# Performance work log

Hardware: AMD Instinct MI355X
Metric: run time of the kernel (lower is better)

Reference implementation:

```python
import jax, jax.numpy as jnp
import numpy as np

NUM_HEAD = 8
GN_GROUPS = 32
EPS = 1e-5


def group_norm(x, w, b):
    # x: [B,C,H,W]; GroupNorm over 32 groups
    B, C, H, W = x.shape
    xg = x.reshape(B, GN_GROUPS, C // GN_GROUPS, H, W)
    mu = jnp.mean(xg, axis=(2, 3, 4), keepdims=True)
    var = jnp.var(xg, axis=(2, 3, 4), keepdims=True)
    xn = ((xg - mu) * jax.lax.rsqrt(var + EPS)).reshape(B, C, H, W)
    return xn * w[None, :, None, None] + b[None, :, None, None]


def conv1x1(x, w, b):
    # 1x1 conv == channel-wise linear: w [O,C], x [B,C,H,W]
    return jnp.einsum('oc,bchw->bohw', w, x) + b[None, :, None, None]


def setup_inputs() -> dict:
    key = jax.random.key(0)
    ks = jax.random.split(key, 6)
    B, C, H, W = 8, 512, 32, 32
    s = 1.0 / np.sqrt(C)
    return {
        'x': jax.random.normal(ks[0], (B, C, H, W), jnp.float32),
        'gn_w': jnp.ones((C,), jnp.float32),
        'gn_b': jnp.zeros((C,), jnp.float32),
        'wq': jax.random.normal(ks[1], (C, C), jnp.float32) * s,
        'bq': jnp.zeros((C,), jnp.float32),
        'wk': jax.random.normal(ks[2], (C, C), jnp.float32) * s,
        'bk': jnp.zeros((C,), jnp.float32),
        'wv': jax.random.normal(ks[3], (C, C), jnp.float32) * s,
        'bv': jnp.zeros((C,), jnp.float32),
        'wo': jax.random.normal(ks[4], (C, C), jnp.float32) * s,
        'bo': jnp.zeros((C,), jnp.float32),
    }


def reference(x, gn_w, gn_b, wq, bq, wk, bk, wv, bv, wo, bo):
    B, C, H, W = x.shape
    Hn = NUM_HEAD
    d = C // Hn
    N = H * W
    scale = d ** -0.5

    xn = group_norm(x, gn_w, gn_b)
    q = conv1x1(xn, wq, bq).reshape(B, Hn, d, N)  # [B,Hn,d,N]
    k = conv1x1(xn, wk, bk).reshape(B, Hn, d, N)
    v = conv1x1(xn, wv, bv).reshape(B, Hn, d, N)

    # attn[b,h,i,j] = sum_d q[b,h,d,i] * k[b,h,d,j]
    attn = jnp.einsum('bhdi,bhdj->bhij', q, k) * scale
    attn = jax.nn.softmax(attn, axis=-1)
    # out[b,h,d,i] = sum_j attn[b,h,i,j] * v[b,h,d,j]
    out = jnp.einsum('bhij,bhdj->bhdi', attn, v).reshape(B, C, H, W)
    return x + conv1x1(out, wo, bo)
```

## Files before the change

### kernel.cpp

```cpp
#include <hip/hip_runtime.h>
#include <hip/hip_bf16.h>

typedef unsigned short ushort_t;
typedef __bf16 bf16_t;
typedef bf16_t bf16x8 __attribute__((ext_vector_type(8)));
typedef float f32x4 __attribute__((ext_vector_type(4)));

#define CH 512
#define NSP 1024

__device__ __forceinline__ float bf2f(ushort_t u) {
    union { unsigned int i; float f; } t; t.i = ((unsigned int)u) << 16; return t.f;
}
__device__ __forceinline__ ushort_t f2bf(float f) {
    union { float fl; unsigned int i; } t; t.fl = f;
    unsigned int r = t.i + 0x7fffu + ((t.i >> 16) & 1u);
    return (ushort_t)(r >> 16);
}
__device__ __forceinline__ unsigned int pk2(float a, float b) {
    __hip_bfloat162 h = __float22bfloat162_rn(make_float2(a, b));
    union { __hip_bfloat162 h2; unsigned int u; } t; t.h2 = h; return t.u;
}

#if __has_builtin(__builtin_amdgcn_global_load_lds)
#define HAVE_ASYNC_LDS 1
#endif
__device__ __forceinline__ void cp16(const ushort_t* g, ushort_t* l) {
#ifdef HAVE_ASYNC_LDS
    __builtin_amdgcn_global_load_lds((const __attribute__((address_space(1))) unsigned int*)g,
                                     (__attribute__((address_space(3))) unsigned int*)l, 16, 0, 0);
#else
    *(uint4*)l = *(const uint4*)g;
#endif
}

#define QSCALE 0.18033688011112042f

__global__ __launch_bounds__(256) void prep_kernel(const float* __restrict__ x,
                                                   const float* __restrict__ w0, const float* __restrict__ w1,
                                                   const float* __restrict__ w2, const float* __restrict__ w3,
                                                   float2* __restrict__ gstats, ushort_t* __restrict__ wbf) {
    int tid = threadIdx.x;
    if (blockIdx.x >= 256) {
        int idx = (blockIdx.x - 256) * 256 + tid;
        int my = idx >> 16;
        const float* src = (my == 0) ? w0 : (my == 1) ? w1 : (my == 2) ? w2 : w3;
        float4 v = reinterpret_cast<const float4*>(src)[idx & 65535];
        uint2 u = make_uint2(pk2(v.x, v.y), pk2(v.z, v.w));
        reinterpret_cast<uint2*>(wbf + (size_t)my * 262144)[idx & 65535] = u;
        return;
    }
    __shared__ float red[8];
    int bg = blockIdx.x;
    size_t base = (size_t)bg * 16384;
    float s = 0.f, s2 = 0.f;
    const float4* x4 = reinterpret_cast<const float4*>(x + base);
    for (int i = tid; i < 4096; i += 256) {
        float4 v = x4[i];
        s  += v.x + v.y + v.z + v.w;
        s2 += v.x * v.x + v.y * v.y + v.z * v.z + v.w * v.w;
    }
    #pragma unroll
    for (int off = 32; off > 0; off >>= 1) {
        s  += __shfl_down(s, off, 64);
        s2 += __shfl_down(s2, off, 64);
    }
    int wv = tid >> 6;
    if ((tid & 63) == 0) { red[wv] = s; red[4 + wv] = s2; }
    __syncthreads();
    if (tid == 0) {
        float ts  = red[0] + red[1] + red[2] + red[3];
        float ts2 = red[4] + red[5] + red[6] + red[7];
        float mu  = ts * (1.f / 16384.f);
        float var = ts2 * (1.f / 16384.f) - mu * mu;
        gstats[bg] = make_float2(mu, rsqrtf(var + 1e-5f));
    }
}

__global__ __launch_bounds__(256) void gn_apply(const float* __restrict__ x, const float* __restrict__ gw,
                                                const float* __restrict__ gbias, const float2* __restrict__ gstats,
                                                ushort_t* __restrict__ xnt) {
    __shared__ __align__(16) ushort_t lt[16 * 264];
    int nq = blockIdx.x;
    int bg = blockIdx.y;
    int b = bg >> 5, g = bg & 31;
    int tid = threadIdx.x;
    float2 st = gstats[bg];
    float mu = st.x, rstd = st.y;
    const float4* x4 = reinterpret_cast<const float4*>(x + ((size_t)(b * 512 + g * 16) * 1024 + nq * 256));
    #pragma unroll
    for (int rep = 0; rep < 4; rep++) {
        int id = rep * 256 + tid;
        int cc = id >> 6, j = id & 63;
        float ww = gw[g * 16 + cc], bb = gbias[g * 16 + cc];
        float ca = rstd * ww, cb = bb - mu * ca;
        float4 v = x4[cc * 256 + j];
        uint2 u = make_uint2(pk2(v.x * ca + cb, v.y * ca + cb), pk2(v.z * ca + cb, v.w * ca + cb));
        *reinterpret_cast<uint2*>(&lt[cc * 264 + j * 4]) = u;
    }
    __syncthreads();
    int n = tid;
    ushort_t ov[16];
    #pragma unroll
    for (int cc = 0; cc < 16; cc++) ov[cc] = lt[cc * 264 + n];
    ushort_t* dst = xnt + ((size_t)(b * 1024 + nq * 256 + n)) * 512 + g * 16;
    *reinterpret_cast<ushort4*>(dst + 0)  = *reinterpret_cast<ushort4*>(&ov[0]);
    *reinterpret_cast<ushort4*>(dst + 4)  = *reinterpret_cast<ushort4*>(&ov[4]);
    *reinterpret_cast<ushort4*>(dst + 8)  = *reinterpret_cast<ushort4*>(&ov[8]);
    *reinterpret_cast<ushort4*>(dst + 12) = *reinterpret_cast<ushort4*>(&ov[12]);
}

__global__ __launch_bounds__(256) void conv_qkv(const ushort_t* __restrict__ xnt,
                                                const ushort_t* __restrict__ wbf,
                                                const float* __restrict__ bq,
                                                const float* __restrict__ bk,
                                                const float* __restrict__ bv,
                                                ushort_t* __restrict__ qt,
                                                ushort_t* __restrict__ kt,
                                                ushort_t* __restrict__ vt) {
    __shared__ __align__(16) char smem[17408];
    ushort_t* als = (ushort_t*)smem;
    ushort_t* bls = (ushort_t*)(smem + 8192);
    int tid = threadIdx.x;
    int wave = tid >> 6, lane = tid & 63, l15 = lane & 15, quad = lane >> 4;
    int wm = wave >> 1, wn = wave & 1;
    int m0 = blockIdx.x * 128, o0 = blockIdx.y * 64, b = blockIdx.z;
    const ushort_t* A = xnt + (size_t)b * 524288;

    f32x4 acc[4][2];
    #pragma unroll
    for (int ms = 0; ms < 4; ms++)
        #pragma unroll
        for (int ns = 0; ns < 2; ns++) acc[ms][ns] = (f32x4){0.f, 0.f, 0.f, 0.f};

    for (int k0 = 0; k0 < 512; k0 += 32) {
        #pragma unroll
        for (int rep = 0; rep < 2; rep++) {
            int id = rep * 256 + tid;
            int r = id >> 2, part = id & 3;
            int sw = part ^ ((r >> 2) & 3);
            cp16(A + (size_t)(m0 + r) * 512 + k0 + sw * 8, als + (size_t)id * 8);
        }
        {
            int r = tid >> 2, part = tid & 3;
            int sw = part ^ ((r >> 2) & 3);
            cp16(wbf + (size_t)(o0 + r) * 512 + k0 + sw * 8, bls + (size_t)tid * 8);
        }
        __syncthreads();
        bf16x8 af[4], bfr[2];
        #pragma unroll
        for (int ms = 0; ms < 4; ms++) {
            int row = wm * 64 + ms * 16 + l15;
            int slot = quad ^ ((row >> 2) & 3);
            af[ms] = *(const bf16x8*)(als + row * 32 + slot * 8);
        }
        #pragma unroll
        for (int ns = 0; ns < 2; ns++) {
            int row = wn * 32 + ns * 16 + l15;
            int slot = quad ^ ((row >> 2) & 3);
            bfr[ns] = *(const bf16x8*)(bls + row * 32 + slot * 8);
        }
        #pragma unroll
        for (int ms = 0; ms < 4; ms++)
            #pragma unroll
            for (int ns = 0; ns < 2; ns++)
                acc[ms][ns] = __builtin_amdgcn_mfma_f32_16x16x32_bf16(af[ms], bfr[ns], acc[ms][ns], 0, 0, 0);
        __syncthreads();
    }

    int seg = o0 >> 9, lo = o0 & 511;
    if (seg < 2) {
        const float* bias = seg ? bk : bq;
        ushort_t* dst = seg ? kt : qt;
        float s = seg ? 1.f : QSCALE;
        float bv0 = bias[lo + wn * 32 + l15];
        float bv1 = bias[lo + wn * 32 + 16 + l15];
        ushort_t* cls = (ushort_t*)smem;
        #pragma unroll
        for (int ms = 0; ms < 4; ms++)
            #pragma unroll
            for (int ns = 0; ns < 2; ns++) {
                float bb = ns ? bv1 : bv0;
                int idx = (wm * 64 + ms * 16 + quad * 4) * 64 + wn * 32 + ns * 16 + l15;
                unsigned int ua = pk2((acc[ms][ns][0] + bb) * s, (acc[ms][ns][1] + bb) * s);
                unsigned int ub = pk2((acc[ms][ns][2] + bb) * s, (acc[ms][ns][3] + bb) * s);
                cls[idx]       = (ushort_t)(ua & 0xffff);
                cls[idx + 64]  = (ushort_t)(ua >> 16);
                cls[idx + 128] = (ushort_t)(ub & 0xffff);
                cls[idx + 192] = (ushort_t)(ub >> 16);
            }
        __syncthreads();
        int h = lo >> 6;
        size_t obase = ((size_t)(b * 8 + h) * 1024 + m0) * 64;
        #pragma unroll
        for (int rep = 0; rep < 4; rep++) {
            int id = rep * 256 + tid;
            int r = id >> 3, part = id & 7;
            *(uint4*)(dst + obase + (size_t)r * 64 + part * 8) = *(const uint4*)(cls + r * 64 + part * 8);
        }
    } else {
        float bv0 = bv[lo + wn * 32 + l15];
        float bv1 = bv[lo + wn * 32 + 16 + l15];
        ushort_t* clst = (ushort_t*)smem;
        #pragma unroll
        for (int ms = 0; ms < 4; ms++)
            #pragma unroll
            for (int ns = 0; ns < 2; ns++) {
                float bb = ns ? bv1 : bv0;
                unsigned int ua = pk2(acc[ms][ns][0] + bb, acc[ms][ns][1] + bb);
                unsigned int ub = pk2(acc[ms][ns][2] + bb, acc[ms][ns][3] + bb);
                *(uint2*)(&clst[(wn * 32 + ns * 16 + l15) * 136 + wm * 64 + ms * 16 + quad * 4]) =
                    make_uint2(ua, ub);
            }
        __syncthreads();
        #pragma unroll
        for (int rep = 0; rep < 4; rep++) {
            int id = rep * 256 + tid;
            int row = id >> 4, part = id & 15;
            *(uint4*)(vt + ((size_t)(b * 512 + lo + row) * 1024 + m0 + part * 8)) =
                *(const uint4*)(clst + row * 136 + part * 8);
        }
    }
}

__global__ __launch_bounds__(256) void attn_kernel(const ushort_t* __restrict__ qt,
                                                   const ushort_t* __restrict__ kt,
                                                   const ushort_t* __restrict__ vt,
                                                   ushort_t* __restrict__ ao) {
    __shared__ __align__(16) ushort_t kls[64 * 72];
    __shared__ __align__(16) ushort_t vls[64 * 72];
    __shared__ __align__(16) ushort_t pls[64 * 88];
    int tid = threadIdx.x;
    int wave = tid >> 6, lane = tid & 63, l15 = lane & 15, quad = lane >> 4;
    int id = blockIdx.x;
    int sub = id >> 3;
    int bh = (id & 7) * 8 + (sub >> 4);
    int i0 = (sub & 15) * 64;
    const ushort_t* qb = qt + (size_t)bh * 65536;
    const ushort_t* kb = kt + (size_t)bh * 65536;
    const ushort_t* vb = vt + (size_t)bh * 65536;
    int iw = wave * 16;

    bf16x8 qf0 = *(const bf16x8*)(qb + (size_t)(i0 + iw + l15) * 64 + quad * 8);
    bf16x8 qf1 = *(const bf16x8*)(qb + (size_t)(i0 + iw + l15) * 64 + 32 + quad * 8);

    f32x4 oacc[4];
    #pragma unroll
    for (int ds = 0; ds < 4; ds++) oacc[ds] = (f32x4){0.f, 0.f, 0.f, 0.f};
    float lacc = 0.f;

    int rl0 = tid >> 3, p0 = tid & 7;
    int rl1 = 32 + rl0;
    uint4 kr0 = *(const uint4*)(kb + (size_t)rl0 * 64 + p0 * 8);
    uint4 kr1 = *(const uint4*)(kb + (size_t)rl1 * 64 + p0 * 8);
    uint4 vr0 = *(const uint4*)(vb + (size_t)rl0 * 1024 + p0 * 8);
    uint4 vr1 = *(const uint4*)(vb + (size_t)rl1 * 1024 + p0 * 8);

    for (int jt = 0; jt < 16; jt++) {
        if (jt) __syncthreads();
        *(uint4*)(kls + rl0 * 72 + p0 * 8) = kr0;
        *(uint4*)(kls + rl1 * 72 + p0 * 8) = kr1;
        *(uint4*)(vls + rl0 * 72 + p0 * 8) = vr0;
        *(uint4*)(vls + rl1 * 72 + p0 * 8) = vr1;
        __syncthreads();
        if (jt < 15) {
            int j0n = (jt + 1) * 64;
            kr0 = *(const uint4*)(kb + (size_t)(j0n + rl0) * 64 + p0 * 8);
            kr1 = *(const uint4*)(kb + (size_t)(j0n + rl1) * 64 + p0 * 8);
            vr0 = *(const uint4*)(vb + (size_t)rl0 * 1024 + j0n + p0 * 8);
            vr1 = *(const uint4*)(vb + (size_t)rl1 * 1024 + j0n + p0 * 8);
        }

        #pragma unroll
        for (int js = 0; js < 4; js++) {
            bf16x8 kf0 = *(const bf16x8*)(kls + (js * 16 + l15) * 72 + quad * 8);
            bf16x8 kf1 = *(const bf16x8*)(kls + (js * 16 + l15) * 72 + 32 + quad * 8);
            f32x4 z = (f32x4){0.f, 0.f, 0.f, 0.f};
            z = __builtin_amdgcn_mfma_f32_16x16x32_bf16(kf0, qf0, z, 0, 0, 0);
            z = __builtin_amdgcn_mfma_f32_16x16x32_bf16(kf1, qf1, z, 0, 0, 0);
            float e0 = exp2f(z[0]), e1 = exp2f(z[1]), e2 = exp2f(z[2]), e3 = exp2f(z[3]);
            lacc += (e0 + e1) + (e2 + e3);
            *(uint2*)(pls + (iw + l15) * 88 + js * 16 + quad * 4) =
                make_uint2(pk2(e0, e1), pk2(e2, e3));
        }
        bf16x8 pa0 = *(const bf16x8*)(pls + (iw + l15) * 88 + quad * 8);
        bf16x8 pa1 = *(const bf16x8*)(pls + (iw + l15) * 88 + 32 + quad * 8);
        #pragma unroll
        for (int ds = 0; ds < 4; ds++) {
            bf16x8 vf0 = *(const bf16x8*)(vls + (ds * 16 + l15) * 72 + quad * 8);
            bf16x8 vf1 = *(const bf16x8*)(vls + (ds * 16 + l15) * 72 + 32 + quad * 8);
            oacc[ds] = __builtin_amdgcn_mfma_f32_16x16x32_bf16(pa0, vf0, oacc[ds], 0, 0, 0);
            oacc[ds] = __builtin_amdgcn_mfma_f32_16x16x32_bf16(pa1, vf1, oacc[ds], 0, 0, 0);
        }
    }

    lacc += __shfl_xor(lacc, 16, 64);
    lacc += __shfl_xor(lacc, 32, 64);
    float linv[4];
    #pragma unroll
    for (int r = 0; r < 4; r++) linv[r] = 1.f / __shfl(lacc, quad * 4 + r, 64);

    __syncthreads();
    #pragma unroll
    for (int ds = 0; ds < 4; ds++)
        #pragma unroll
        for (int r = 0; r < 4; r++)
            kls[(iw + quad * 4 + r) * 72 + ds * 16 + l15] = f2bf(oacc[ds][r] * linv[r]);
    __syncthreads();
    int b = bh >> 3, h = bh & 7;
    ushort_t* aob = ao + ((size_t)b * 1024 + i0) * 512 + h * 64;
    #pragma unroll
    for (int rep = 0; rep < 2; rep++) {
        int idd = rep * 256 + tid;
        int rl = idd >> 3, part = idd & 7;
        *(uint4*)(aob + (size_t)rl * 512 + part * 8) = *(const uint4*)(kls + rl * 72 + part * 8);
    }
}

__global__ __launch_bounds__(256) void conv_out(const ushort_t* __restrict__ ao,
                                                const ushort_t* __restrict__ wo,
                                                const float* __restrict__ bo,
                                                const float* __restrict__ xres,
                                                float* __restrict__ out) {
    __shared__ __align__(16) char smem[17408];
    ushort_t* als = (ushort_t*)smem;
    ushort_t* bls = (ushort_t*)(smem + 4096);
    int tid = threadIdx.x;
    int wave = tid >> 6, lane = tid & 63, l15 = lane & 15, quad = lane >> 4;
    int wm = wave >> 1, wn = wave & 1;
    int m0 = blockIdx.x * 64, n0 = blockIdx.y * 64, b = blockIdx.z;
    const ushort_t* B = ao + (size_t)b * 524288;

    f32x4 acc[2][2];
    #pragma unroll
    for (int ms = 0; ms < 2; ms++)
        #pragma unroll
        for (int ns = 0; ns < 2; ns++) acc[ms][ns] = (f32x4){0.f, 0.f, 0.f, 0.f};

    for (int k0 = 0; k0 < 512; k0 += 32) {
        {
            int r = tid >> 2, part = tid & 3;
            int sw = part ^ ((r >> 2) & 3);
            cp16(wo + (size_t)(m0 + r) * 512 + k0 + sw * 8, als + (size_t)tid * 8);
            cp16(B + (size_t)(n0 + r) * 512 + k0 + sw * 8, bls + (size_t)tid * 8);
        }
        __syncthreads();
        bf16x8 af[2], bfr[2];
        #pragma unroll
        for (int ms = 0; ms < 2; ms++) {
            int row = wm * 32 + ms * 16 + l15;
            int slot = quad ^ ((row >> 2) & 3);
            af[ms] = *(const bf16x8*)(als + row * 32 + slot * 8);
        }
        #pragma unroll
        for (int ns = 0; ns < 2; ns++) {
            int row = wn * 32 + ns * 16 + l15;
            int slot = quad ^ ((row >> 2) & 3);
            bfr[ns] = *(const bf16x8*)(bls + row * 32 + slot * 8);
        }
        #pragma unroll
        for (int ms = 0; ms < 2; ms++)
            #pragma unroll
            for (int ns = 0; ns < 2; ns++)
                acc[ms][ns] = __builtin_amdgcn_mfma_f32_16x16x32_bf16(af[ms], bfr[ns], acc[ms][ns], 0, 0, 0);
        __syncthreads();
    }

    float* clsf = (float*)smem;
    #pragma unroll
    for (int ms = 0; ms < 2; ms++)
        #pragma unroll
        for (int ns = 0; ns < 2; ns++)
            #pragma unroll
            for (int r = 0; r < 4; r++)
                clsf[(wm * 32 + ms * 16 + quad * 4 + r) * 68 + wn * 32 + ns * 16 + l15] = acc[ms][ns][r];
    __syncthreads();
    #pragma unroll
    for (int rep = 0; rep < 4; rep++) {
        int id = rep * 256 + tid;
        int row = id >> 4, part = id & 15;
        float bvr = bo[m0 + row];
        float4 c4 = *(const float4*)(clsf + row * 68 + part * 4);
        size_t ga = ((size_t)(b * 512 + m0 + row)) * 1024 + n0 + part * 4;
        float4 xv = *(const float4*)(xres + ga);
        c4.x += bvr + xv.x; c4.y += bvr + xv.y; c4.z += bvr + xv.z; c4.w += bvr + xv.w;
        *(float4*)(out + ga) = c4;
    }
}

extern "C" void kernel_launch(void* const* d_in, const int* in_sizes, int n_in,
                              void* d_out, int out_size, void* d_ws, size_t ws_size,
                              hipStream_t stream) {
    const float* x    = (const float*)d_in[0];
    const float* gn_w = (const float*)d_in[1];
    const float* gn_b = (const float*)d_in[2];
    const float* wq   = (const float*)d_in[3];
    const float* bq   = (const float*)d_in[4];
    const float* wk   = (const float*)d_in[5];
    const float* bk   = (const float*)d_in[6];
    const float* wv   = (const float*)d_in[7];
    const float* bv   = (const float*)d_in[8];
    const float* wo   = (const float*)d_in[9];
    const float* bo   = (const float*)d_in[10];

    char* ws = (char*)d_ws;
    ushort_t* xnt  = (ushort_t*)(ws);
    ushort_t* qt   = (ushort_t*)(ws + (((size_t)8)  << 20));
    ushort_t* kt   = (ushort_t*)(ws + (((size_t)16) << 20));
    ushort_t* vt   = (ushort_t*)(ws + (((size_t)24) << 20));
    ushort_t* wbf  = (ushort_t*)(ws + (((size_t)32) << 20));
    float2*   gst  = (float2*)  (ws + (((size_t)34) << 20));
    ushort_t* ao   = xnt;

    prep_kernel<<<1280, 256, 0, stream>>>(x, wq, wk, wv, wo, gst, wbf);
    gn_apply<<<dim3(4, 256), 256, 0, stream>>>(x, gn_w, gn_b, gst, xnt);

    conv_qkv<<<dim3(8, 24, 8), 256, 0, stream>>>(xnt, wbf, bq, bk, bv, qt, kt, vt);

    attn_kernel<<<1024, 256, 0, stream>>>(qt, kt, vt, ao);

    conv_out<<<dim3(8, 16, 8), 256, 0, stream>>>(ao, wbf + 786432, bo, x, (float*)d_out);
}
```

Baseline: 175.7 us.

## Rewrite attention with 32x32 MFMA, register-resident P, async double-buffered K/V

The attention kernel now uses 32x32x16 bf16 MFMAs, with 128 query rows per block and 32 per wave, which halves the grid to 512 blocks. The probability tile stays in registers and is rearranged with v_permlane32_swap instead of a round trip through LDS. K/V tiles are loaded with async global-to-LDS copies into a double buffer with an XOR-swizzled layout, and the native exp2 is used. This aims to cut LDS traffic, sync count and instruction overhead, at the cost of fewer blocks (less occupancy and parallelism) and more register pressure.

```diff
diff --git a/kernel.cpp b/kernel.cpp
--- a/kernel.cpp
+++ b/kernel.cpp
@@ -5,6 +5,7 @@
 typedef __bf16 bf16_t;
 typedef bf16_t bf16x8 __attribute__((ext_vector_type(8)));
 typedef float f32x4 __attribute__((ext_vector_type(4)));
+typedef float f32x16 __attribute__((ext_vector_type(16)));
 
 #define CH 512
 #define NSP 1024
@@ -33,6 +34,12 @@
     *(uint4*)l = *(const uint4*)g;
 #endif
 }
+
+#if __has_builtin(__builtin_amdgcn_exp2f)
+#define EXP2(x) __builtin_amdgcn_exp2f(x)
+#else
+#define EXP2(x) exp2f(x)
+#endif
 
 #define QSCALE 0.18033688011112042f
 
@@ -223,97 +230,135 @@
     }
 }
 
+#define Z16 {0.f,0.f,0.f,0.f,0.f,0.f,0.f,0.f,0.f,0.f,0.f,0.f,0.f,0.f,0.f,0.f}
+
+#define PV_STEP(JS, P) {                                                                     \
+    unsigned wA0 = pk2(P[((JS)&1)*8+0], P[((JS)&1)*8+1]);                                    \
+    unsigned wA1 = pk2(P[((JS)&1)*8+2], P[((JS)&1)*8+3]);                                    \
+    unsigned wB0 = pk2(P[((JS)&1)*8+4], P[((JS)&1)*8+5]);                                    \
+    unsigned wB1 = pk2(P[((JS)&1)*8+6], P[((JS)&1)*8+7]);                                    \
+    asm("v_permlane32_swap_b32 %0, %1" : "+v"(wA0), "+v"(wB0));                              \
+    asm("v_permlane32_swap_b32 %0, %1" : "+v"(wA1), "+v"(wB1));                              \
+    union { unsigned u[4]; bf16x8 v; } pa_;                                                  \
+    pa_.u[0] = wA0; pa_.u[1] = wA1; pa_.u[2] = wB0; pa_.u[3] = wB1;                          \
+    int phys_ = (((JS) * 2) | hi) ^ r7;                                                      \
+    bf16x8 vf0 = *(const bf16x8*)(vbuf + l31 * 64 + phys_ * 8);                              \
+    bf16x8 vf1 = *(const bf16x8*)(vbuf + (32 + l31) * 64 + phys_ * 8);                       \
+    __builtin_amdgcn_s_setprio(1);                                                           \
+    vacc0 = __builtin_amdgcn_mfma_f32_32x32x16_bf16(pa_.v, vf0, vacc0, 0, 0, 0);             \
+    vacc1 = __builtin_amdgcn_mfma_f32_32x32x16_bf16(pa_.v, vf1, vacc1, 0, 0, 0);             \
+    __builtin_amdgcn_s_setprio(0); }
+
 __global__ __launch_bounds__(256) void attn_kernel(const ushort_t* __restrict__ qt,
                                                    const ushort_t* __restrict__ kt,
                                                    const ushort_t* __restrict__ vt,
                                                    ushort_t* __restrict__ ao) {
-    __shared__ __align__(16) ushort_t kls[64 * 72];
-    __shared__ __align__(16) ushort_t vls[64 * 72];
-    __shared__ __align__(16) ushort_t pls[64 * 88];
+    __shared__ __align__(16) ushort_t smem[16384];
     int tid = threadIdx.x;
-    int wave = tid >> 6, lane = tid & 63, l15 = lane & 15, quad = lane >> 4;
+    int wave = tid >> 6, lane = tid & 63, l31 = lane & 31, hi = lane >> 5;
     int id = blockIdx.x;
-    int sub = id >> 3;
-    int bh = (id & 7) * 8 + (sub >> 4);
-    int i0 = (sub & 15) * 64;
+    int bh = (id & 7) * 8 + (id >> 6);
+    int i0 = ((id >> 3) & 7) * 128;
     const ushort_t* qb = qt + (size_t)bh * 65536;
     const ushort_t* kb = kt + (size_t)bh * 65536;
     const ushort_t* vb = vt + (size_t)bh * 65536;
-    int iw = wave * 16;
-
-    bf16x8 qf0 = *(const bf16x8*)(qb + (size_t)(i0 + iw + l15) * 64 + quad * 8);
-    bf16x8 qf1 = *(const bf16x8*)(qb + (size_t)(i0 + iw + l15) * 64 + 32 + quad * 8);
-
-    f32x4 oacc[4];
-    #pragma unroll
-    for (int ds = 0; ds < 4; ds++) oacc[ds] = (f32x4){0.f, 0.f, 0.f, 0.f};
+    int iw0 = i0 + wave * 32;
+    int r7 = l31 & 7;
+
+    bf16x8 qf[4];
+    #pragma unroll
+    for (int ks = 0; ks < 4; ks++)
+        qf[ks] = *(const bf16x8*)(qb + (size_t)(iw0 + l31) * 64 + ks * 16 + hi * 8);
+
+    f32x16 vacc0 = Z16, vacc1 = Z16;
     float lacc = 0.f;
 
-    int rl0 = tid >> 3, p0 = tid & 7;
-    int rl1 = 32 + rl0;
-    uint4 kr0 = *(const uint4*)(kb + (size_t)rl0 * 64 + p0 * 8);
-    uint4 kr1 = *(const uint4*)(kb + (size_t)rl1 * 64 + p0 * 8);
-    uint4 vr0 = *(const uint4*)(vb + (size_t)rl0 * 1024 + p0 * 8);
-    uint4 vr1 = *(const uint4*)(vb + (size_t)rl1 * 1024 + p0 * 8);
+    int rk0 = tid >> 3, sk = tid & 7, rk1 = rk0 + 32;
+    const ushort_t* kg0 = kb + rk0 * 64 + (sk ^ (rk0 & 7)) * 8;
+    const ushort_t* kg1 = kb + rk1 * 64 + (sk ^ (rk1 & 7)) * 8;
+    const ushort_t* vg0 = vb + (size_t)rk0 * 1024 + (sk ^ (rk0 & 7)) * 8;
+    const ushort_t* vg1 = vb + (size_t)rk1 * 1024 + (sk ^ (rk1 & 7)) * 8;
+
+    cp16(kg0, smem + tid * 8);
+    cp16(kg1, smem + (tid + 256) * 8);
+    cp16(vg0, smem + 8192 + tid * 8);
+    cp16(vg1, smem + 8192 + (tid + 256) * 8);
+    kg0 += 4096; kg1 += 4096; vg0 += 64; vg1 += 64;
+    __syncthreads();
 
     for (int jt = 0; jt < 16; jt++) {
-        if (jt) __syncthreads();
-        *(uint4*)(kls + rl0 * 72 + p0 * 8) = kr0;
-        *(uint4*)(kls + rl1 * 72 + p0 * 8) = kr1;
-        *(uint4*)(vls + rl0 * 72 + p0 * 8) = vr0;
-        *(uint4*)(vls + rl1 * 72 + p0 * 8) = vr1;
-        __syncthreads();
+        int cur = jt & 1;
         if (jt < 15) {
-            int j0n = (jt + 1) * 64;
-            kr0 = *(const uint4*)(kb + (size_t)(j0n + rl0) * 64 + p0 * 8);
-            kr1 = *(const uint4*)(kb + (size_t)(j0n + rl1) * 64 + p0 * 8);
-            vr0 = *(const uint4*)(vb + (size_t)rl0 * 1024 + j0n + p0 * 8);
-            vr1 = *(const uint4*)(vb + (size_t)rl1 * 1024 + j0n + p0 * 8);
-        }
-
-        #pragma unroll
-        for (int js = 0; js < 4; js++) {
-            bf16x8 kf0 = *(const bf16x8*)(kls + (js * 16 + l15) * 72 + quad * 8);
-            bf16x8 kf1 = *(const bf16x8*)(kls + (js * 16 + l15) * 72 + 32 + quad * 8);
-            f32x4 z = (f32x4){0.f, 0.f, 0.f, 0.f};
-            z = __builtin_amdgcn_mfma_f32_16x16x32_bf16(kf0, qf0, z, 0, 0, 0);
-            z = __builtin_amdgcn_mfma_f32_16x16x32_bf16(kf1, qf1, z, 0, 0, 0);
-            float e0 = exp2f(z[0]), e1 = exp2f(z[1]), e2 = exp2f(z[2]), e3 = exp2f(z[3]);
-            lacc += (e0 + e1) + (e2 + e3);
-            *(uint2*)(pls + (iw + l15) * 88 + js * 16 + quad * 4) =
-                make_uint2(pk2(e0, e1), pk2(e2, e3));
-        }
-        bf16x8 pa0 = *(const bf16x8*)(pls + (iw + l15) * 88 + quad * 8);
-        bf16x8 pa1 = *(const bf16x8*)(pls + (iw + l15) * 88 + 32 + quad * 8);
-        #pragma unroll
-        for (int ds = 0; ds < 4; ds++) {
-            bf16x8 vf0 = *(const bf16x8*)(vls + (ds * 16 + l15) * 72 + quad * 8);
-            bf16x8 vf1 = *(const bf16x8*)(vls + (ds * 16 + l15) * 72 + 32 + quad * 8);
-            oacc[ds] = __builtin_amdgcn_mfma_f32_16x16x32_bf16(pa0, vf0, oacc[ds], 0, 0, 0);
-            oacc[ds] = __builtin_amdgcn_mfma_f32_16x16x32_bf16(pa1, vf1, oacc[ds], 0, 0, 0);
-        }
-    }
-
-    lacc += __shfl_xor(lacc, 16, 64);
+            ushort_t* kd = smem + (cur ^ 1) * 4096;
+            ushort_t* vd = smem + 8192 + (cur ^ 1) * 4096;
+            cp16(kg0, kd + tid * 8);
+            cp16(kg1, kd + (tid + 256) * 8);
+            cp16(vg0, vd + tid * 8);
+            cp16(vg1, vd + (tid + 256) * 8);
+            kg0 += 4096; kg1 += 4096; vg0 += 64; vg1 += 64;
+        }
+        const ushort_t* kbuf = smem + cur * 4096;
+        const ushort_t* vbuf = smem + 8192 + cur * 4096;
+
+        f32x16 s0 = Z16, s1 = Z16;
+        __builtin_amdgcn_s_setprio(1);
+        #pragma unroll
+        for (int ks = 0; ks < 4; ks++) {
+            int phys = ((ks * 2) | hi) ^ r7;
+            bf16x8 kf = *(const bf16x8*)(kbuf + l31 * 64 + phys * 8);
+            s0 = __builtin_amdgcn_mfma_f32_32x32x16_bf16(kf, qf[ks], s0, 0, 0, 0);
+        }
+        #pragma unroll
+        for (int ks = 0; ks < 4; ks++) {
+            int phys = ((ks * 2) | hi) ^ r7;
+            bf16x8 kf = *(const bf16x8*)(kbuf + (32 + l31) * 64 + phys * 8);
+            s1 = __builtin_amdgcn_mfma_f32_32x32x16_bf16(kf, qf[ks], s1, 0, 0, 0);
+        }
+        __builtin_amdgcn_s_setprio(0);
+
+        float p0[16], p1[16];
+        #pragma unroll
+        for (int r = 0; r < 16; r++) p0[r] = EXP2(s0[r]);
+        #pragma unroll
+        for (int r = 0; r < 16; r++) p1[r] = EXP2(s1[r]);
+        float t0 = 0.f, t1 = 0.f, t2 = 0.f, t3 = 0.f;
+        #pragma unroll
+        for (int r = 0; r < 4; r++) { t0 += p0[r]; t1 += p0[4 + r]; t2 += p0[8 + r]; t3 += p0[12 + r]; }
+        #pragma unroll
+        for (int r = 0; r < 4; r++) { t0 += p1[r]; t1 += p1[4 + r]; t2 += p1[8 + r]; t3 += p1[12 + r]; }
+        lacc += (t0 + t1) + (t2 + t3);
+
+        PV_STEP(0, p0)
+        PV_STEP(1, p0)
+        PV_STEP(2, p1)
+        PV_STEP(3, p1)
+
+        __syncthreads();
+    }
+
     lacc += __shfl_xor(lacc, 32, 64);
-    float linv[4];
-    #pragma unroll
-    for (int r = 0; r < 4; r++) linv[r] = 1.f / __shfl(lacc, quad * 4 + r, 64);
-
-    __syncthreads();
-    #pragma unroll
-    for (int ds = 0; ds < 4; ds++)
-        #pragma unroll
-        for (int r = 0; r < 4; r++)
-            kls[(iw + quad * 4 + r) * 72 + ds * 16 + l15] = f2bf(oacc[ds][r] * linv[r]);
+    float linv[16];
+    #pragma unroll
+    for (int r = 0; r < 16; r++) {
+        int ir = (r & 3) + 8 * (r >> 2) + 4 * hi;
+        linv[r] = 1.f / __shfl(lacc, ir, 64);
+    }
+
+    ushort_t* ols = smem;
+    #pragma unroll
+    for (int r = 0; r < 16; r++) {
+        int irow = wave * 32 + (r & 3) + 8 * (r >> 2) + 4 * hi;
+        ols[irow * 80 + l31]      = f2bf(vacc0[r] * linv[r]);
+        ols[irow * 80 + 32 + l31] = f2bf(vacc1[r] * linv[r]);
+    }
     __syncthreads();
     int b = bh >> 3, h = bh & 7;
     ushort_t* aob = ao + ((size_t)b * 1024 + i0) * 512 + h * 64;
     #pragma unroll
-    for (int rep = 0; rep < 2; rep++) {
+    for (int rep = 0; rep < 4; rep++) {
         int idd = rep * 256 + tid;
         int rl = idd >> 3, part = idd & 7;
-        *(uint4*)(aob + (size_t)rl * 512 + part * 8) = *(const uint4*)(kls + rl * 72 + part * 8);
+        *(uint4*)(aob + (size_t)rl * 512 + part * 8) = *(const uint4*)(ols + rl * 80 + part * 8);
     }
 }
 
@@ -417,7 +462,7 @@
 
     conv_qkv<<<dim3(8, 24, 8), 256, 0, stream>>>(xnt, wbf, bq, bk, bv, qt, kt, vt);
 
-    attn_kernel<<<1024, 256, 0, stream>>>(qt, kt, vt, ao);
+    attn_kernel<<<512, 256, 0, stream>>>(qt, kt, vt, ao);
 
     conv_out<<<dim3(8, 16, 8), 256, 0, stream>>>(ao, wbf + 786432, bo, x, (float*)d_out);
 }
```

New measurement: 167.1 us. 1.05x faster.
